# Kernel optimization log

Hardware: AMD Instinct MI355X
Metric: run time of the kernel (lower is better)

The kernel has to match this reference:

```python
import jax, jax.numpy as jnp
import numpy as np

B, IN, HID, OUT = 1024, 256, 512, 2
MU_INIT, LOGVAR_INIT = 0.0, -5.0
VAR_MIN = 1e-6


def setup_inputs() -> dict:
    key = jax.random.key(0)
    ks = jax.random.split(key, 9)
    inp = {
        "x": jax.random.normal(ks[0], (B, IN), dtype=jnp.float32),
        "w1_mu": MU_INIT + 0.1 * jax.random.normal(ks[1], (HID, IN), dtype=jnp.float32),
        "w1_logvar": LOGVAR_INIT + 0.1 * jax.random.normal(ks[2], (HID, IN), dtype=jnp.float32),
        "b1_mu": MU_INIT + 0.1 * jax.random.normal(ks[3], (HID,), dtype=jnp.float32),
        "b1_logvar": LOGVAR_INIT + 0.1 * jax.random.normal(ks[4], (HID,), dtype=jnp.float32),
        "w2_mu": MU_INIT + 0.1 * jax.random.normal(ks[5], (OUT, HID), dtype=jnp.float32),
        "w2_logvar": LOGVAR_INIT + 0.1 * jax.random.normal(ks[6], (OUT, HID), dtype=jnp.float32),
        "b2_mu": MU_INIT + 0.1 * jax.random.normal(ks[7], (OUT,), dtype=jnp.float32),
        "b2_logvar": LOGVAR_INIT + 0.1 * jax.random.normal(ks[8], (OUT,), dtype=jnp.float32),
    }
    return inp


def _bayes_linear(x, w_mu, w_logvar, b_mu, b_logvar, eps_w, eps_b):
    # Non-efficient path: per-example sampled weights (batch, out, in) and biases (batch, out)
    w_std = jnp.exp(0.5 * w_logvar)
    b_std = jnp.exp(0.5 * b_logvar)
    weights = w_mu[None, :, :] + w_std[None, :, :] * eps_w  # (B, O, I)
    biases = b_mu[None, :] + b_std[None, :] * eps_b          # (B, O)
    out = jnp.einsum("boi,bi->bo", weights, x)
    return out + biases


def reference(x, w1_mu, w1_logvar, b1_mu, b1_logvar, w2_mu, w2_logvar, b2_mu, b2_logvar):
    # Noise sampled inside forward, matching torch.randn in the module (fixed key for determinism)
    nk = jax.random.split(jax.random.key(42), 4)
    eps_w1 = jax.random.normal(nk[0], (B, HID, IN), dtype=x.dtype)
    eps_b1 = jax.random.normal(nk[1], (B, HID), dtype=x.dtype)
    eps_w2 = jax.random.normal(nk[2], (B, OUT, HID), dtype=x.dtype)
    eps_b2 = jax.random.normal(nk[3], (B, OUT), dtype=x.dtype)

    h = jax.nn.relu(_bayes_linear(x, w1_mu, w1_logvar, b1_mu, b1_logvar, eps_w1, eps_b1))
    out = _bayes_linear(h, w2_mu, w2_logvar, b2_mu, b2_logvar, eps_w2, eps_b2)  # (B, 2)
    mean = out[:, 0]
    var = jnp.maximum(jnp.exp(out[:, 1]), VAR_MIN)
    return mean, var
```

## Files before the change

kernel.cpp:

```cpp
#include <hip/hip_runtime.h>
#include <stdint.h>

#define BATCH 1024
#define IN    256
#define HID   512
#define OUT   2

#define SQRT2 1.4142135623730951

__host__ __device__ __forceinline__ uint32_t rotl32(uint32_t x, uint32_t r) {
#ifdef __HIP_DEVICE_COMPILE__
    return __builtin_rotateleft32(x, r);
#else
    return (x << r) | (x >> (32 - r));
#endif
}

__host__ __device__ __forceinline__ void threefry2x32(uint32_t k0, uint32_t k1,
                                                      uint32_t& x0, uint32_t& x1) {
    uint32_t k2 = k0 ^ k1 ^ 0x1BD11BDAu;
    x0 += k0; x1 += k1;
#define TF_R(r) { x0 += x1; x1 = rotl32(x1, (r)); x1 ^= x0; }
    TF_R(13) TF_R(15) TF_R(26) TF_R(6)   x0 += k1; x1 += k2 + 1u;
    TF_R(17) TF_R(29) TF_R(16) TF_R(24)  x0 += k2; x1 += k0 + 2u;
    TF_R(13) TF_R(15) TF_R(26) TF_R(6)   x0 += k0; x1 += k1 + 3u;
    TF_R(17) TF_R(29) TF_R(16) TF_R(24)  x0 += k1; x1 += k2 + 4u;
    TF_R(13) TF_R(15) TF_R(26) TF_R(6)   x0 += k2; x1 += k0 + 5u;
#undef TF_R
}

struct TFK {
    uint32_t k0, k1, k2, i1b, i2b, i3b, i4b, i5b;
    uint32_t k1j0, k1j1, k1j2, k1j3;
    uint32_t K01j0, K01j1, K01j2, K01j3;
    __device__ __forceinline__ TFK(uint32_t a, uint32_t b) {
        k0 = a; k1 = b; k2 = a ^ b ^ 0x1BD11BDAu;
        i1b = k2 + 1u; i2b = k0 + 2u; i3b = k1 + 3u; i4b = k2 + 4u; i5b = k0 + 5u;
        k1j0 = k1;        k1j1 = k1 + 1u;   k1j2 = k1 + 2u;   k1j3 = k1 + 3u;
        uint32_t K01 = k0 + k1;
        K01j0 = K01;      K01j1 = K01 + 1u; K01j2 = K01 + 2u; K01j3 = K01 + 3u;
    }
};

__device__ __forceinline__ uint32_t tf_core(const TFK& K, uint32_t cnt,
                                            uint32_t k1j, uint32_t K01j) {
    uint32_t t  = cnt + k1j;
    uint32_t x0 = cnt + K01j;
    uint32_t x1 = rotl32(t, 13) ^ x0;
    x0 += x1; x1 = rotl32(x1, 15) ^ x0;
    x0 += x1; x1 = rotl32(x1, 26) ^ x0;
    x0 += x1; x1 = rotl32(x1,  6) ^ x0;
    t = x1 + K.i1b; x0 = x0 + t + K.k1;  x1 = rotl32(t, 17) ^ x0;
    x0 += x1; x1 = rotl32(x1, 29) ^ x0;
    x0 += x1; x1 = rotl32(x1, 16) ^ x0;
    x0 += x1; x1 = rotl32(x1, 24) ^ x0;
    t = x1 + K.i2b; x0 = x0 + t + K.k2;  x1 = rotl32(t, 13) ^ x0;
    x0 += x1; x1 = rotl32(x1, 15) ^ x0;
    x0 += x1; x1 = rotl32(x1, 26) ^ x0;
    x0 += x1; x1 = rotl32(x1,  6) ^ x0;
    t = x1 + K.i3b; x0 = x0 + t + K.k0;  x1 = rotl32(t, 17) ^ x0;
    x0 += x1; x1 = rotl32(x1, 29) ^ x0;
    x0 += x1; x1 = rotl32(x1, 16) ^ x0;
    x0 += x1; x1 = rotl32(x1, 24) ^ x0;
    t = x1 + K.i4b; x0 = x0 + t + K.k1;  x1 = rotl32(t, 13) ^ x0;
    x0 += x1; x1 = rotl32(x1, 15) ^ x0;
    x0 += x1; x1 = rotl32(x1, 26) ^ x0;
    x0 += x1; x1 = rotl32(x1,  6) ^ x0;
    return (x0 + K.k2) ^ (x1 + K.i5b);
}
__device__ __forceinline__ uint32_t tf_bits(const TFK& K, uint32_t cnt) {
    return tf_core(K, cnt, K.k1j0, K.K01j0);
}

__device__ __forceinline__ float bits_to_normal(uint32_t bits) {
    const float LO = -0.99999994f;
#if __has_builtin(__builtin_amdgcn_alignbit)
    float m = __uint_as_float(__builtin_amdgcn_alignbit(0x7Fu, bits, 9u));
#else
    float m = __uint_as_float((bits >> 9) | 0x3f800000u);
#endif
    float u = fmaxf(LO, fmaf(m, 2.0f, -3.0f));
    float z = fmaf(-u, u, 1.0f);
    float L = __log2f(z);
    float wa = fmaf(L, -0.69314718f, -2.5f);
    float p = (float)(0.00021858087 * SQRT2);
    p = fmaf(p, wa, (float)(-0.00125372503 * SQRT2));
    p = fmaf(p, wa, (float)(-0.00417768164 * SQRT2));
    p = fmaf(p, wa, (float)(0.246640727 * SQRT2));
    p = fmaf(p, wa, (float)(1.50140941 * SQRT2));
    return p * u;
}

__global__ __launch_bounds__(256) void k_w1std(const float* __restrict__ w1_logvar,
                                               float* __restrict__ w1_std) {
    int i = blockIdx.x * 256 + threadIdx.x;
    if (i < HID * IN) w1_std[i] = __expf(0.5f * w1_logvar[i]);
}

__global__ __launch_bounds__(256, 4) void k_layer1(
    const float* __restrict__ x, const float* __restrict__ w1_mu,
    const float* __restrict__ w1_std, const float* __restrict__ b1_mu,
    const float* __restrict__ b1_logvar,
    const float* __restrict__ w2_mu, const float* __restrict__ w2_logvar,
    float* __restrict__ partials,
    uint32_t kw0, uint32_t kw1, uint32_t kb0, uint32_t kb1,
    uint32_t k2w0, uint32_t k2w1)
{
    __shared__ float xs[IN];
    __shared__ float red[8];
    const int b = blockIdx.y;
    const int o = blockIdx.x * 256 + threadIdx.x;
    xs[threadIdx.x] = x[b * IN + threadIdx.x];
    __syncthreads();

    const TFK Kw(kw0, kw1);
    const float4* wm4 = (const float4*)(w1_mu  + o * IN);
    const float4* ws4 = (const float4*)(w1_std + o * IN);
    const float4* x4  = (const float4*)xs;

    uint32_t c = (uint32_t)(b * HID + o) * IN;
    float acc = 0.f;

    float4 m4 = wm4[0], s4 = ws4[0], xv = x4[0];
    #pragma unroll 3
    for (int i4 = 0; i4 < IN / 4 - 1; ++i4) {
        float4 m4n = wm4[i4 + 1], s4n = ws4[i4 + 1], xvn = x4[i4 + 1];
        float e0 = bits_to_normal(tf_core(Kw, c, Kw.k1j0, Kw.K01j0));
        float e1 = bits_to_normal(tf_core(Kw, c, Kw.k1j1, Kw.K01j1));
        float e2 = bits_to_normal(tf_core(Kw, c, Kw.k1j2, Kw.K01j2));
        float e3 = bits_to_normal(tf_core(Kw, c, Kw.k1j3, Kw.K01j3));
        c += 4u;
        acc = fmaf(fmaf(s4.x, e0, m4.x), xv.x, acc);
        acc = fmaf(fmaf(s4.y, e1, m4.y), xv.y, acc);
        acc = fmaf(fmaf(s4.z, e2, m4.z), xv.z, acc);
        acc = fmaf(fmaf(s4.w, e3, m4.w), xv.w, acc);
        m4 = m4n; s4 = s4n; xv = xvn;
    }
    {
        float e0 = bits_to_normal(tf_core(Kw, c, Kw.k1j0, Kw.K01j0));
        float e1 = bits_to_normal(tf_core(Kw, c, Kw.k1j1, Kw.K01j1));
        float e2 = bits_to_normal(tf_core(Kw, c, Kw.k1j2, Kw.K01j2));
        float e3 = bits_to_normal(tf_core(Kw, c, Kw.k1j3, Kw.K01j3));
        acc = fmaf(fmaf(s4.x, e0, m4.x), xv.x, acc);
        acc = fmaf(fmaf(s4.y, e1, m4.y), xv.y, acc);
        acc = fmaf(fmaf(s4.z, e2, m4.z), xv.z, acc);
        acc = fmaf(fmaf(s4.w, e3, m4.w), xv.w, acc);
    }
    const TFK Kb(kb0, kb1);
    float eb = bits_to_normal(tf_bits(Kb, (uint32_t)(b * HID + o)));
    float hv = fmaxf(acc + fmaf(__expf(0.5f * b1_logvar[o]), eb, b1_mu[o]), 0.f);

    const TFK K2(k2w0, k2w1);
    uint32_t c2 = (uint32_t)(b * OUT) * HID + (uint32_t)o;
    float e20 = bits_to_normal(tf_bits(K2, c2));
    float e21 = bits_to_normal(tf_bits(K2, c2 + HID));
    float a0 = fmaf(__expf(0.5f * w2_logvar[o]),       e20, w2_mu[o])       * hv;
    float a1 = fmaf(__expf(0.5f * w2_logvar[HID + o]), e21, w2_mu[HID + o]) * hv;

    #pragma unroll
    for (int off = 32; off > 0; off >>= 1) {
        a0 += __shfl_down(a0, off, 64);
        a1 += __shfl_down(a1, off, 64);
    }
    const int wv = threadIdx.x >> 6, ln = threadIdx.x & 63;
    if (ln == 0) { red[wv] = a0; red[4 + wv] = a1; }
    __syncthreads();
    if (threadIdx.x == 0) {
        float* p = partials + ((size_t)blockIdx.x * BATCH + b) * 2;
        p[0] = (red[0] + red[1]) + (red[2] + red[3]);
        p[1] = (red[4] + red[5]) + (red[6] + red[7]);
    }
}

__global__ __launch_bounds__(256) void k_epilogue(
    const float* __restrict__ partials, const float* __restrict__ b2_mu,
    const float* __restrict__ b2_logvar, float* __restrict__ out,
    uint32_t kb0, uint32_t kb1)
{
    const int t = blockIdx.x * 256 + threadIdx.x;
    const int b = t >> 1, j = t & 1;
    float v = partials[((size_t)0 * BATCH + b) * 2 + j]
            + partials[((size_t)1 * BATCH + b) * 2 + j];
    const TFK Kb(kb0, kb1);
    float eb = bits_to_normal(tf_bits(Kb, (uint32_t)(b * OUT + j)));
    float o0 = v + fmaf(__expf(0.5f * b2_logvar[j]), eb, b2_mu[j]);
    if (j == 0) out[b] = o0;
    else        out[1024 + b] = fmaxf(__expf(o0), 1e-6f);
}

extern "C" void kernel_launch(void* const* d_in, const int* in_sizes, int n_in,
                              void* d_out, int out_size, void* d_ws, size_t ws_size,
                              hipStream_t stream) {
    (void)in_sizes; (void)n_in; (void)out_size; (void)ws_size;
    const float* x         = (const float*)d_in[0];
    const float* w1_mu     = (const float*)d_in[1];
    const float* w1_logvar = (const float*)d_in[2];
    const float* b1_mu     = (const float*)d_in[3];
    const float* b1_logvar = (const float*)d_in[4];
    const float* w2_mu     = (const float*)d_in[5];
    const float* w2_logvar = (const float*)d_in[6];
    const float* b2_mu     = (const float*)d_in[7];
    const float* b2_logvar = (const float*)d_in[8];
    float* out = (float*)d_out;

    float* ws_w1std = (float*)d_ws;
    float* ws_part  = (float*)d_ws + HID * IN;

    uint32_t nk[4][2];
    for (uint32_t i = 0; i < 4; ++i) {
        uint32_t a = 0u, c = i;
        threefry2x32(0u, 42u, a, c);
        nk[i][0] = a; nk[i][1] = c;
    }
    const uint32_t kw1a = nk[0][0], kw1b = nk[0][1];
    const uint32_t kb1a = nk[1][0], kb1b = nk[1][1];
    const uint32_t kw2a = nk[2][0], kw2b = nk[2][1];
    const uint32_t kb2a = nk[3][0], kb2b = nk[3][1];

    k_w1std<<<(HID * IN + 255) / 256, 256, 0, stream>>>(w1_logvar, ws_w1std);
    k_layer1<<<dim3(2, 1024), 256, 0, stream>>>(x, w1_mu, ws_w1std, b1_mu, b1_logvar,
                                                w2_mu, w2_logvar, ws_part,
                                                kw1a, kw1b, kb1a, kb1b, kw2a, kw2b);
    k_epilogue<<<8, 256, 0, stream>>>(ws_part, b2_mu, b2_logvar, out, kb2a, kb2b);
}
```

Baseline: 316.4 us.

## Fuse layer-1 and epilogue into one kernel per batch row, simplify inverse-erf polynomial

Each 512-thread block now handles one batch row across all hidden units, reducing both output columns in shared memory and applying the second-layer bias and exp directly. This drops the partials buffer and the separate epilogue launch. The inverse-erf polynomial is refit in terms of log2 directly, with sqrt2 folded into the coefficients, which saves an FMA per sample. Launch bounds move from (256,4) to (512,8), which may raise register pressure on the heavy threefry loop, and the refit polynomial may change numerical accuracy.

```diff
diff --git a/kernel.cpp b/kernel.cpp
--- a/kernel.cpp
+++ b/kernel.cpp
@@ -5,8 +5,6 @@
 #define IN    256
 #define HID   512
 #define OUT   2
-
-#define SQRT2 1.4142135623730951
 
 __host__ __device__ __forceinline__ uint32_t rotl32(uint32_t x, uint32_t r) {
 #ifdef __HIP_DEVICE_COMPILE__
@@ -82,12 +80,11 @@
     float u = fmaxf(LO, fmaf(m, 2.0f, -3.0f));
     float z = fmaf(-u, u, 1.0f);
     float L = __log2f(z);
-    float wa = fmaf(L, -0.69314718f, -2.5f);
-    float p = (float)(0.00021858087 * SQRT2);
-    p = fmaf(p, wa, (float)(-0.00125372503 * SQRT2));
-    p = fmaf(p, wa, (float)(-0.00417768164 * SQRT2));
-    p = fmaf(p, wa, (float)(0.246640727 * SQRT2));
-    p = fmaf(p, wa, (float)(1.50140941 * SQRT2));
+    float p = 7.1356100e-05f;
+    p = fmaf(p, L, 1.6199146e-03f);
+    p = fmaf(p, L, 9.1198018e-03f);
+    p = fmaf(p, L, -0.22581331f);
+    p = fmaf(p, L, 1.2541575f);
     return p * u;
 }
 
@@ -97,20 +94,21 @@
     if (i < HID * IN) w1_std[i] = __expf(0.5f * w1_logvar[i]);
 }
 
-__global__ __launch_bounds__(256, 4) void k_layer1(
+__global__ __launch_bounds__(512, 8) void k_fused(
     const float* __restrict__ x, const float* __restrict__ w1_mu,
     const float* __restrict__ w1_std, const float* __restrict__ b1_mu,
     const float* __restrict__ b1_logvar,
     const float* __restrict__ w2_mu, const float* __restrict__ w2_logvar,
-    float* __restrict__ partials,
+    const float* __restrict__ b2_mu, const float* __restrict__ b2_logvar,
+    float* __restrict__ out,
     uint32_t kw0, uint32_t kw1, uint32_t kb0, uint32_t kb1,
-    uint32_t k2w0, uint32_t k2w1)
+    uint32_t k2w0, uint32_t k2w1, uint32_t k2b0, uint32_t k2b1)
 {
     __shared__ float xs[IN];
-    __shared__ float red[8];
-    const int b = blockIdx.y;
-    const int o = blockIdx.x * 256 + threadIdx.x;
-    xs[threadIdx.x] = x[b * IN + threadIdx.x];
+    __shared__ float red[16];
+    const int b = blockIdx.x;
+    const int o = threadIdx.x;
+    if (o < IN) xs[o] = x[b * IN + o];
     __syncthreads();
 
     const TFK Kw(kw0, kw1);
@@ -162,30 +160,19 @@
         a0 += __shfl_down(a0, off, 64);
         a1 += __shfl_down(a1, off, 64);
     }
-    const int wv = threadIdx.x >> 6, ln = threadIdx.x & 63;
-    if (ln == 0) { red[wv] = a0; red[4 + wv] = a1; }
+    const int wv = o >> 6, ln = o & 63;
+    if (ln == 0) { red[wv] = a0; red[8 + wv] = a1; }
     __syncthreads();
-    if (threadIdx.x == 0) {
-        float* p = partials + ((size_t)blockIdx.x * BATCH + b) * 2;
-        p[0] = (red[0] + red[1]) + (red[2] + red[3]);
-        p[1] = (red[4] + red[5]) + (red[6] + red[7]);
-    }
-}
-
-__global__ __launch_bounds__(256) void k_epilogue(
-    const float* __restrict__ partials, const float* __restrict__ b2_mu,
-    const float* __restrict__ b2_logvar, float* __restrict__ out,
-    uint32_t kb0, uint32_t kb1)
-{
-    const int t = blockIdx.x * 256 + threadIdx.x;
-    const int b = t >> 1, j = t & 1;
-    float v = partials[((size_t)0 * BATCH + b) * 2 + j]
-            + partials[((size_t)1 * BATCH + b) * 2 + j];
-    const TFK Kb(kb0, kb1);
-    float eb = bits_to_normal(tf_bits(Kb, (uint32_t)(b * OUT + j)));
-    float o0 = v + fmaf(__expf(0.5f * b2_logvar[j]), eb, b2_mu[j]);
-    if (j == 0) out[b] = o0;
-    else        out[1024 + b] = fmaxf(__expf(o0), 1e-6f);
+    if (o < 2) {
+        const float* r = red + o * 8;
+        float v = ((r[0] + r[1]) + (r[2] + r[3]))
+                + ((r[4] + r[5]) + (r[6] + r[7]));
+        const TFK Kb2(k2b0, k2b1);
+        float eb2 = bits_to_normal(tf_bits(Kb2, (uint32_t)(b * OUT + o)));
+        float oo = v + fmaf(__expf(0.5f * b2_logvar[o]), eb2, b2_mu[o]);
+        if (o == 0) out[b] = oo;
+        else        out[1024 + b] = fmaxf(__expf(oo), 1e-6f);
+    }
 }
 
 extern "C" void kernel_launch(void* const* d_in, const int* in_sizes, int n_in,
@@ -204,7 +191,6 @@
     float* out = (float*)d_out;
 
     float* ws_w1std = (float*)d_ws;
-    float* ws_part  = (float*)d_ws + HID * IN;
 
     uint32_t nk[4][2];
     for (uint32_t i = 0; i < 4; ++i) {
@@ -218,8 +204,8 @@
     const uint32_t kb2a = nk[3][0], kb2b = nk[3][1];
 
     k_w1std<<<(HID * IN + 255) / 256, 256, 0, stream>>>(w1_logvar, ws_w1std);
-    k_layer1<<<dim3(2, 1024), 256, 0, stream>>>(x, w1_mu, ws_w1std, b1_mu, b1_logvar,
-                                                w2_mu, w2_logvar, ws_part,
-                                                kw1a, kw1b, kb1a, kb1b, kw2a, kw2b);
-    k_epilogue<<<8, 256, 0, stream>>>(ws_part, b2_mu, b2_logvar, out, kb2a, kb2b);
-}
+    k_fused<<<1024, 512, 0, stream>>>(x, w1_mu, ws_w1std, b1_mu, b1_logvar,
+                                      w2_mu, w2_logvar, b2_mu, b2_logvar, out,
+                                      kw1a, kw1b, kb1a, kb1b,
+                                      kw2a, kw2b, kb2a, kb2b);
+}
```

New measurement: 317.7 us. No clear change (+0.4%).
